# Optimization experiments

Hardware: AMD Instinct MI355X
Metric: run time of the kernel (lower is better)

## Reference

```python
import jax, jax.numpy as jnp
import numpy as np

ALPHA = 1.0
BETA = 1.0
N, D, C = 131072, 512, 1000


def setup_inputs() -> dict:
    key = jax.random.key(0)
    k1, k2, k3 = jax.random.split(key, 3)
    feat = jax.random.normal(k1, (N, D), dtype=jnp.float32)
    classifier = jax.random.normal(k2, (C, D), dtype=jnp.float32)
    target = jax.random.randint(k3, (N,), 0, C, dtype=jnp.int64)
    return {"feat": feat, "classifier": classifier, "target": target}


def reference(feat, classifier, target):
    # --- weight-wise MHE term ---
    w = classifier / jnp.linalg.norm(classifier, axis=1, keepdims=True)  # [C, D]
    sq = jnp.sum(w * w, axis=1)  # [C]
    d2 = jnp.maximum(sq[:, None] + sq[None, :] - 2.0 * (w @ w.T), 0.0)  # [C, C] squared dists
    # triu(diagonal=1) then mask >0  <=>  upper-triangular strictly positive entries
    triu = jnp.triu(jnp.ones((C, C), dtype=bool), k=1)
    mask = triu & (d2 > 0)
    safe_d2 = jnp.where(mask, d2, 1.0)
    # mean of 1/d^2 over masked entries (1/(d*d) == 1/d2)
    weight_wise = jnp.sum(jnp.where(mask, 1.0 / safe_d2, 0.0)) / jnp.sum(mask)

    # --- sample-wise concentration term (per-class mean of dist to its weight) ---
    feat_n = feat / jnp.linalg.norm(feat, axis=1, keepdims=True)  # [N, D]
    w_t = jax.lax.stop_gradient(w)[target]  # [N, D], class mean detached
    dist = jnp.linalg.norm(feat_n - w_t, axis=1)  # [N] cdist to a single point
    counts = jax.ops.segment_sum(jnp.ones_like(dist), target, num_segments=C)  # [C]
    sums = jax.ops.segment_sum(dist, target, num_segments=C)  # [C]
    present = counts > 0
    class_means = jnp.where(present, sums / jnp.maximum(counts, 1.0), 0.0)
    sample_wise_all = jnp.sum(class_means) / jnp.sum(present)

    return (sample_wise_all * BETA, weight_wise * ALPHA, feat)
```

## Files before the change

### kernel.cpp

```cpp
#include <hip/hip_runtime.h>
#include <hip/hip_bf16.h>

#define NN 131072
#define DD 512
#define CC 1000


__device__ __forceinline__ float wave_reduce(float v) {
#pragma unroll
    for (int m = 32; m > 0; m >>= 1) v += __shfl_xor(v, m, 64);
    return v;
}

__global__ __launch_bounds__(64) void knorm(const float* __restrict__ cls,
                                            float* __restrict__ w,
                                            float* __restrict__ sqw) {
    int c = blockIdx.x;
    int lane = threadIdx.x;
    const float4* src = (const float4*)(cls + (size_t)c * DD) + lane * 2;
    float4 f0 = src[0], f1 = src[1];
    float s = f0.x * f0.x + f0.y * f0.y + f0.z * f0.z + f0.w * f0.w +
              f1.x * f1.x + f1.y * f1.y + f1.z * f1.z + f1.w * f1.w;
    s = wave_reduce(s);
    float inv = rsqrtf(s);
    float4 w0 = make_float4(f0.x * inv, f0.y * inv, f0.z * inv, f0.w * inv);
    float4 w1 = make_float4(f1.x * inv, f1.y * inv, f1.z * inv, f1.w * inv);
    float q = w0.x * w0.x + w0.y * w0.y + w0.z * w0.z + w0.w * w0.w +
              w1.x * w1.x + w1.y * w1.y + w1.z * w1.z + w1.w * w1.w;
    q = wave_reduce(q);
    float4* dst = (float4*)(w + (size_t)c * DD) + lane * 2;
    dst[0] = w0;
    dst[1] = w1;
    if (lane == 0) sqw[c] = q;
}

#define TILE 32
#define KC 64
__global__ __launch_bounds__(256) void kpair(const float* __restrict__ w,
                                             const float* __restrict__ sqw,
                                             float* __restrict__ pair_acc) {
    int bi = blockIdx.y, bj = blockIdx.x;
    if (bj < bi) return;

    __shared__ float As[TILE][KC + 1];
    __shared__ float Bs[TILE][KC + 1];

    int tid = threadIdx.x;
    int tx = tid & 15, ty = tid >> 4;
    int lrow = tid >> 3;
    int lcol = (tid & 7) * 8;
    int i0 = bi * TILE, j0 = bj * TILE;

    float acc00 = 0.f, acc01 = 0.f, acc10 = 0.f, acc11 = 0.f;

    for (int k0 = 0; k0 < DD; k0 += KC) {
        {
            int gi = i0 + lrow;
            float4 v0 = make_float4(0, 0, 0, 0), v1 = v0;
            if (gi < CC) {
                const float4* p = (const float4*)(w + (size_t)gi * DD + k0 + lcol);
                v0 = p[0]; v1 = p[1];
            }
            As[lrow][lcol + 0] = v0.x; As[lrow][lcol + 1] = v0.y;
            As[lrow][lcol + 2] = v0.z; As[lrow][lcol + 3] = v0.w;
            As[lrow][lcol + 4] = v1.x; As[lrow][lcol + 5] = v1.y;
            As[lrow][lcol + 6] = v1.z; As[lrow][lcol + 7] = v1.w;

            int gj = j0 + lrow;
            v0 = make_float4(0, 0, 0, 0); v1 = v0;
            if (gj < CC) {
                const float4* p = (const float4*)(w + (size_t)gj * DD + k0 + lcol);
                v0 = p[0]; v1 = p[1];
            }
            Bs[lrow][lcol + 0] = v0.x; Bs[lrow][lcol + 1] = v0.y;
            Bs[lrow][lcol + 2] = v0.z; Bs[lrow][lcol + 3] = v0.w;
            Bs[lrow][lcol + 4] = v1.x; Bs[lrow][lcol + 5] = v1.y;
            Bs[lrow][lcol + 6] = v1.z; Bs[lrow][lcol + 7] = v1.w;
        }
        __syncthreads();
#pragma unroll
        for (int k = 0; k < KC; ++k) {
            float a0 = As[2 * ty + 0][k];
            float a1 = As[2 * ty + 1][k];
            float b0 = Bs[2 * tx + 0][k];
            float b1 = Bs[2 * tx + 1][k];
            acc00 += a0 * b0; acc01 += a0 * b1;
            acc10 += a1 * b0; acc11 += a1 * b1;
        }
        __syncthreads();
    }

    float lsum = 0.f, lcnt = 0.f;
    int i_ = i0 + 2 * ty, j_ = j0 + 2 * tx;
    {
        int ii[2] = {i_, i_ + 1};
        int jj[2] = {j_, j_ + 1};
        float d[2][2] = {{acc00, acc01}, {acc10, acc11}};
#pragma unroll
        for (int a = 0; a < 2; ++a)
#pragma unroll
            for (int b = 0; b < 2; ++b) {
                int i = ii[a], j = jj[b];
                if (i < CC && j < CC && j > i) {
                    float d2 = sqw[i] + sqw[j] - 2.f * d[a][b];
                    if (d2 > 0.f) { lsum += 1.f / d2; lcnt += 1.f; }
                }
            }
    }
    lsum = wave_reduce(lsum);
    lcnt = wave_reduce(lcnt);
    __shared__ float rs[4], rc[4];
    int wv = tid >> 6;
    if ((tid & 63) == 0) { rs[wv] = lsum; rc[wv] = lcnt; }
    __syncthreads();
    if (tid == 0) {
        atomicAdd(pair_acc + 0, rs[0] + rs[1] + rs[2] + rs[3]);
        atomicAdd(pair_acc + 1, rc[0] + rc[1] + rc[2] + rc[3]);
    }
}

__global__ __launch_bounds__(256) void ksample(const float* __restrict__ feat,
                                               const int* __restrict__ target,
                                               const float* __restrict__ w,
                                               const float* __restrict__ sqw,
                                               float* __restrict__ class_sum,
                                               float* __restrict__ class_cnt,
                                               float* __restrict__ out_feat) {
    int t = threadIdx.x;
    int rlocal = t >> 7;
    long long n = (long long)blockIdx.x * 2 + rlocal;
    size_t f4idx = (size_t)blockIdx.x * 256 + t;

    const float4* f4 = (const float4*)feat;
    float4 f = f4[f4idx];

    int tgt = target[n];
    int col4 = t & 127;
    const float4* w4 = (const float4*)w;
    float4 wv = w4[(size_t)tgt * 128 + col4];

    float2* o2 = (float2*)out_feat;
    o2[2 * f4idx] = make_float2(f.x, f.y);
    o2[2 * f4idx + 1] = make_float2(f.z, f.w);

    float ff = f.x * f.x + f.y * f.y + f.z * f.z + f.w * f.w;
    float fw = f.x * wv.x + f.y * wv.y + f.z * wv.z + f.w * wv.w;
#pragma unroll
    for (int m = 32; m > 0; m >>= 1) {
        ff += __shfl_xor(ff, m, 64);
        fw += __shfl_xor(fw, m, 64);
    }

    __shared__ float red[4][2];
    int wid = t >> 6;
    if ((t & 63) == 0) { red[wid][0] = ff; red[wid][1] = fw; }
    __syncthreads();

    if ((t & 127) == 0) {
        int wa = rlocal * 2, wb = rlocal * 2 + 1;
        float sff = red[wa][0] + red[wb][0];
        float sfw = red[wa][1] + red[wb][1];
        float inv = rsqrtf(sff);
        float d2 = sff * inv * inv + sqw[tgt] - 2.f * inv * sfw;
        d2 = fmaxf(d2, 0.f);
        float dist = sqrtf(d2);
        atomicAdd(class_sum + tgt, dist);
        atomicAdd(class_cnt + tgt, 1.f);
    }
}

__global__ __launch_bounds__(256) void kfin(const float* __restrict__ class_sum,
                                            const float* __restrict__ class_cnt,
                                            const float* __restrict__ pair_acc,
                                            float* __restrict__ out) {
    float msum = 0.f, pcnt = 0.f;
    for (int c = threadIdx.x; c < CC; c += 256) {
        float cnt = class_cnt[c];
        if (cnt > 0.f) {
            msum += class_sum[c] / cnt;
            pcnt += 1.f;
        }
    }
    msum = wave_reduce(msum);
    pcnt = wave_reduce(pcnt);
    __shared__ float rs[4], rc[4];
    int wv = threadIdx.x >> 6;
    if ((threadIdx.x & 63) == 0) { rs[wv] = msum; rc[wv] = pcnt; }
    __syncthreads();
    if (threadIdx.x == 0) {
        float sm = rs[0] + rs[1] + rs[2] + rs[3];
        float sp = rc[0] + rc[1] + rc[2] + rc[3];
        out[0] = 1.0f * (sm / sp);
        out[1] = 1.0f * (pair_acc[0] / pair_acc[1]);
    }
}

extern "C" void kernel_launch(void* const* d_in, const int* in_sizes, int n_in,
                              void* d_out, int out_size, void* d_ws, size_t ws_size,
                              hipStream_t stream) {
    const float* feat = (const float*)d_in[0];
    const float* cls = (const float*)d_in[1];
    const int* target = (const int*)d_in[2];
    float* out = (float*)d_out;
    float* ws = (float*)d_ws;

    float* w = ws;
    float* sqw = ws + 512000;
    float* class_sum = ws + 513000;
    float* class_cnt = ws + 514000;
    float* pair_acc = ws + 515000;

    hipMemsetAsync(class_sum, 0, (2 * CC + 2) * sizeof(float), stream);

    knorm<<<CC, 64, 0, stream>>>(cls, w, sqw);
    kpair<<<dim3((CC + TILE - 1) / TILE, (CC + TILE - 1) / TILE), 256, 0, stream>>>(w, sqw, pair_acc);
    ksample<<<NN / 2, 256, 0, stream>>>(feat, target, w, sqw, class_sum, class_cnt, out + 2);
    kfin<<<1, 256, 0, stream>>>(class_sum, class_cnt, pair_acc, out);
}
```

Baseline: 523.2 us.

## Fuse pairwise and sample kernels into one launch with larger register tiles

Merges the pairwise-distance kernel and the per-sample distance kernel into one grid. The first 136 blocks handle upper-triangular 64x64 tiles with 4x4 register blocking and a transposed LDS layout. The remaining blocks each process 8 rows using nontemporal loads and stores, with half-wave reductions. This removes a kernel launch and lets the small pair work overlap the bandwidth-bound feature copy, and it raises arithmetic intensity in the Gram computation. The cost is mixed block types in one grid, and pair blocks use more registers, which may limit occupancy.

```diff
diff --git a/kernel.cpp b/kernel.cpp
--- a/kernel.cpp
+++ b/kernel.cpp
@@ -1,9 +1,18 @@
 #include <hip/hip_runtime.h>
-#include <hip/hip_bf16.h>
 
 #define NN 131072
 #define DD 512
 #define CC 1000
+
+#define CT 64
+#define KCP 32
+#define NTILE 16
+#define NPAIR 136
+#define SROWS 8
+#define NSAMP (NN / SROWS)
+
+typedef float f32x4 __attribute__((ext_vector_type(4)));
+typedef float f32x2 __attribute__((ext_vector_type(2)));
 
 
 __device__ __forceinline__ float wave_reduce(float v) {
@@ -34,137 +43,152 @@
     if (lane == 0) sqw[c] = q;
 }
 
-#define TILE 32
-#define KC 64
-__global__ __launch_bounds__(256) void kpair(const float* __restrict__ w,
+__global__ __launch_bounds__(256) void kmain(const float* __restrict__ feat,
+                                             const int* __restrict__ target,
+                                             const float* __restrict__ w,
                                              const float* __restrict__ sqw,
-                                             float* __restrict__ pair_acc) {
-    int bi = blockIdx.y, bj = blockIdx.x;
-    if (bj < bi) return;
-
-    __shared__ float As[TILE][KC + 1];
-    __shared__ float Bs[TILE][KC + 1];
-
-    int tid = threadIdx.x;
-    int tx = tid & 15, ty = tid >> 4;
-    int lrow = tid >> 3;
-    int lcol = (tid & 7) * 8;
-    int i0 = bi * TILE, j0 = bj * TILE;
-
-    float acc00 = 0.f, acc01 = 0.f, acc10 = 0.f, acc11 = 0.f;
-
-    for (int k0 = 0; k0 < DD; k0 += KC) {
-        {
-            int gi = i0 + lrow;
-            float4 v0 = make_float4(0, 0, 0, 0), v1 = v0;
+                                             float* __restrict__ class_sum,
+                                             float* __restrict__ class_cnt,
+                                             float* __restrict__ pair_acc,
+                                             float* __restrict__ out_feat) {
+    int t = threadIdx.x;
+
+    if (blockIdx.x < NPAIR) {
+        __shared__ float As[KCP][CT + 4];
+        __shared__ float Bs[KCP][CT + 4];
+        __shared__ float rs[4], rc[4];
+
+        int bi = 0, rem = blockIdx.x;
+        while (rem >= NTILE - bi) { rem -= NTILE - bi; ++bi; }
+        int bj = bi + rem;
+        int i0 = bi * CT, j0 = bj * CT;
+
+        int tx = t & 15, ty = t >> 4;
+        int lrow = t >> 2;
+        int kc = (t & 3) * 8;
+
+        float acc[4][4] = {{0.f, 0.f, 0.f, 0.f}};
+
+        for (int k0 = 0; k0 < DD; k0 += KCP) {
+            f32x4 a0 = {0.f, 0.f, 0.f, 0.f}, a1 = a0, b0 = a0, b1 = a0;
+            int gi = i0 + lrow, gj = j0 + lrow;
             if (gi < CC) {
-                const float4* p = (const float4*)(w + (size_t)gi * DD + k0 + lcol);
-                v0 = p[0]; v1 = p[1];
-            }
-            As[lrow][lcol + 0] = v0.x; As[lrow][lcol + 1] = v0.y;
-            As[lrow][lcol + 2] = v0.z; As[lrow][lcol + 3] = v0.w;
-            As[lrow][lcol + 4] = v1.x; As[lrow][lcol + 5] = v1.y;
-            As[lrow][lcol + 6] = v1.z; As[lrow][lcol + 7] = v1.w;
-
-            int gj = j0 + lrow;
-            v0 = make_float4(0, 0, 0, 0); v1 = v0;
+                const f32x4* p = (const f32x4*)(w + (size_t)gi * DD + k0 + kc);
+                a0 = p[0]; a1 = p[1];
+            }
             if (gj < CC) {
-                const float4* p = (const float4*)(w + (size_t)gj * DD + k0 + lcol);
-                v0 = p[0]; v1 = p[1];
-            }
-            Bs[lrow][lcol + 0] = v0.x; Bs[lrow][lcol + 1] = v0.y;
-            Bs[lrow][lcol + 2] = v0.z; Bs[lrow][lcol + 3] = v0.w;
-            Bs[lrow][lcol + 4] = v1.x; Bs[lrow][lcol + 5] = v1.y;
-            Bs[lrow][lcol + 6] = v1.z; Bs[lrow][lcol + 7] = v1.w;
-        }
-        __syncthreads();
-#pragma unroll
-        for (int k = 0; k < KC; ++k) {
-            float a0 = As[2 * ty + 0][k];
-            float a1 = As[2 * ty + 1][k];
-            float b0 = Bs[2 * tx + 0][k];
-            float b1 = Bs[2 * tx + 1][k];
-            acc00 += a0 * b0; acc01 += a0 * b1;
-            acc10 += a1 * b0; acc11 += a1 * b1;
-        }
-        __syncthreads();
-    }
-
-    float lsum = 0.f, lcnt = 0.f;
-    int i_ = i0 + 2 * ty, j_ = j0 + 2 * tx;
-    {
-        int ii[2] = {i_, i_ + 1};
-        int jj[2] = {j_, j_ + 1};
-        float d[2][2] = {{acc00, acc01}, {acc10, acc11}};
-#pragma unroll
-        for (int a = 0; a < 2; ++a)
-#pragma unroll
-            for (int b = 0; b < 2; ++b) {
-                int i = ii[a], j = jj[b];
-                if (i < CC && j < CC && j > i) {
-                    float d2 = sqw[i] + sqw[j] - 2.f * d[a][b];
+                const f32x4* p = (const f32x4*)(w + (size_t)gj * DD + k0 + kc);
+                b0 = p[0]; b1 = p[1];
+            }
+            __syncthreads();
+            As[kc + 0][lrow] = a0.x; As[kc + 1][lrow] = a0.y;
+            As[kc + 2][lrow] = a0.z; As[kc + 3][lrow] = a0.w;
+            As[kc + 4][lrow] = a1.x; As[kc + 5][lrow] = a1.y;
+            As[kc + 6][lrow] = a1.z; As[kc + 7][lrow] = a1.w;
+            Bs[kc + 0][lrow] = b0.x; Bs[kc + 1][lrow] = b0.y;
+            Bs[kc + 2][lrow] = b0.z; Bs[kc + 3][lrow] = b0.w;
+            Bs[kc + 4][lrow] = b1.x; Bs[kc + 5][lrow] = b1.y;
+            Bs[kc + 6][lrow] = b1.z; Bs[kc + 7][lrow] = b1.w;
+            __syncthreads();
+#pragma unroll
+            for (int k = 0; k < KCP; ++k) {
+                f32x4 av = *(const f32x4*)&As[k][4 * ty];
+                f32x4 bv = *(const f32x4*)&Bs[k][4 * tx];
+#pragma unroll
+                for (int a = 0; a < 4; ++a)
+#pragma unroll
+                    for (int b = 0; b < 4; ++b)
+                        acc[a][b] += av[a] * bv[b];
+            }
+        }
+
+        float lsum = 0.f, lcnt = 0.f;
+        int ib = i0 + 4 * ty, jb = j0 + 4 * tx;
+#pragma unroll
+        for (int a = 0; a < 4; ++a)
+#pragma unroll
+            for (int b = 0; b < 4; ++b) {
+                int i = ib + a, j = jb + b;
+                if (j > i && j < CC) {
+                    float d2 = sqw[i] + sqw[j] - 2.f * acc[a][b];
                     if (d2 > 0.f) { lsum += 1.f / d2; lcnt += 1.f; }
                 }
             }
-    }
-    lsum = wave_reduce(lsum);
-    lcnt = wave_reduce(lcnt);
-    __shared__ float rs[4], rc[4];
-    int wv = tid >> 6;
-    if ((tid & 63) == 0) { rs[wv] = lsum; rc[wv] = lcnt; }
+        lsum = wave_reduce(lsum);
+        lcnt = wave_reduce(lcnt);
+        int wv = t >> 6;
+        if ((t & 63) == 0) { rs[wv] = lsum; rc[wv] = lcnt; }
+        __syncthreads();
+        if (t == 0) {
+            atomicAdd(pair_acc + 0, rs[0] + rs[1] + rs[2] + rs[3]);
+            atomicAdd(pair_acc + 1, rc[0] + rc[1] + rc[2] + rc[3]);
+        }
+        return;
+    }
+
+    __shared__ float red[8][4][2];
+    long long n0 = (long long)(blockIdx.x - NPAIR) * SROWS;
+    int col4 = t & 127;
+    int rhalf = t >> 7;
+
+    const f32x4* f4 = (const f32x4*)feat;
+    const f32x4* w4 = (const f32x4*)w;
+    f32x2* o2 = (f32x2*)out_feat;
+
+    int tg[4];
+#pragma unroll
+    for (int i = 0; i < 4; ++i) tg[i] = target[n0 + rhalf + 2 * i];
+
+    size_t fi[4];
+    f32x4 f[4];
+#pragma unroll
+    for (int i = 0; i < 4; ++i) {
+        fi[i] = (size_t)(n0 + rhalf + 2 * i) * 128 + col4;
+        f[i] = __builtin_nontemporal_load(f4 + fi[i]);
+    }
+
+    f32x4 wv[4];
+#pragma unroll
+    for (int i = 0; i < 4; ++i) wv[i] = w4[(size_t)tg[i] * 128 + col4];
+
+#pragma unroll
+    for (int i = 0; i < 4; ++i) {
+        f32x2 lo = {f[i].x, f[i].y}, hi = {f[i].z, f[i].w};
+        __builtin_nontemporal_store(lo, o2 + 2 * fi[i]);
+        __builtin_nontemporal_store(hi, o2 + 2 * fi[i] + 1);
+    }
+
+    float ff[4], fw[4];
+#pragma unroll
+    for (int i = 0; i < 4; ++i) {
+        ff[i] = f[i].x * f[i].x + f[i].y * f[i].y + f[i].z * f[i].z + f[i].w * f[i].w;
+        fw[i] = f[i].x * wv[i].x + f[i].y * wv[i].y + f[i].z * wv[i].z + f[i].w * wv[i].w;
+    }
+#pragma unroll
+    for (int m = 16; m > 0; m >>= 1)
+#pragma unroll
+        for (int i = 0; i < 4; ++i) {
+            ff[i] += __shfl_xor(ff[i], m, 64);
+            fw[i] += __shfl_xor(fw[i], m, 64);
+        }
+    int p = t >> 5;
+    if ((t & 31) == 0) {
+#pragma unroll
+        for (int i = 0; i < 4; ++i) { red[p][i][0] = ff[i]; red[p][i][1] = fw[i]; }
+    }
     __syncthreads();
-    if (tid == 0) {
-        atomicAdd(pair_acc + 0, rs[0] + rs[1] + rs[2] + rs[3]);
-        atomicAdd(pair_acc + 1, rc[0] + rc[1] + rc[2] + rc[3]);
-    }
-}
-
-__global__ __launch_bounds__(256) void ksample(const float* __restrict__ feat,
-                                               const int* __restrict__ target,
-                                               const float* __restrict__ w,
-                                               const float* __restrict__ sqw,
-                                               float* __restrict__ class_sum,
-                                               float* __restrict__ class_cnt,
-                                               float* __restrict__ out_feat) {
-    int t = threadIdx.x;
-    int rlocal = t >> 7;
-    long long n = (long long)blockIdx.x * 2 + rlocal;
-    size_t f4idx = (size_t)blockIdx.x * 256 + t;
-
-    const float4* f4 = (const float4*)feat;
-    float4 f = f4[f4idx];
-
-    int tgt = target[n];
-    int col4 = t & 127;
-    const float4* w4 = (const float4*)w;
-    float4 wv = w4[(size_t)tgt * 128 + col4];
-
-    float2* o2 = (float2*)out_feat;
-    o2[2 * f4idx] = make_float2(f.x, f.y);
-    o2[2 * f4idx + 1] = make_float2(f.z, f.w);
-
-    float ff = f.x * f.x + f.y * f.y + f.z * f.z + f.w * f.w;
-    float fw = f.x * wv.x + f.y * wv.y + f.z * wv.z + f.w * wv.w;
-#pragma unroll
-    for (int m = 32; m > 0; m >>= 1) {
-        ff += __shfl_xor(ff, m, 64);
-        fw += __shfl_xor(fw, m, 64);
-    }
-
-    __shared__ float red[4][2];
-    int wid = t >> 6;
-    if ((t & 63) == 0) { red[wid][0] = ff; red[wid][1] = fw; }
-    __syncthreads();
-
-    if ((t & 127) == 0) {
-        int wa = rlocal * 2, wb = rlocal * 2 + 1;
-        float sff = red[wa][0] + red[wb][0];
-        float sfw = red[wa][1] + red[wb][1];
+    if ((t & 127) < 4) {
+        int i = t & 127;
+        int base = rhalf * 4;
+        float sff = red[base][i][0] + red[base + 1][i][0] +
+                    red[base + 2][i][0] + red[base + 3][i][0];
+        float sfw = red[base][i][1] + red[base + 1][i][1] +
+                    red[base + 2][i][1] + red[base + 3][i][1];
+        int tgt = tg[i];
         float inv = rsqrtf(sff);
         float d2 = sff * inv * inv + sqw[tgt] - 2.f * inv * sfw;
         d2 = fmaxf(d2, 0.f);
-        float dist = sqrtf(d2);
-        atomicAdd(class_sum + tgt, dist);
+        atomicAdd(class_sum + tgt, sqrtf(d2));
         atomicAdd(class_cnt + tgt, 1.f);
     }
 }
@@ -213,7 +237,7 @@
     hipMemsetAsync(class_sum, 0, (2 * CC + 2) * sizeof(float), stream);
 
     knorm<<<CC, 64, 0, stream>>>(cls, w, sqw);
-    kpair<<<dim3((CC + TILE - 1) / TILE, (CC + TILE - 1) / TILE), 256, 0, stream>>>(w, sqw, pair_acc);
-    ksample<<<NN / 2, 256, 0, stream>>>(feat, target, w, sqw, class_sum, class_cnt, out + 2);
+    kmain<<<NPAIR + NSAMP, 256, 0, stream>>>(feat, target, w, sqw,
+                                             class_sum, class_cnt, pair_acc, out + 2);
     kfin<<<1, 256, 0, stream>>>(class_sum, class_cnt, pair_acc, out);
 }
```

Measured after the change: 498.7 us. 1.05x faster.
